# Kernel tuning notes

Hardware: AMD Instinct MI355X
Metric: run time of the kernel (lower is better)

Reference implementation:

```python
import jax, jax.numpy as jnp
import numpy as np

EPS = 1e-6

def setup_inputs() -> dict:
    key = jax.random.key(0)
    M, N, D = 6, 4096, 512
    output = jax.random.normal(key, (M, N, D), dtype=jnp.float32)
    return {"output": output}

def reference(output):
    # output: [M, N, D] stacked per-layer features (already flatten(1)'d)
    M, N, _ = output.shape
    # Gram matrices K_i = X_i @ X_i^T with zeroed diagonal: [M, N, N]
    K = jnp.einsum('ind,imd->inm', output, output)
    K = K * (1.0 - jnp.eye(N, dtype=K.dtype))
    # Double centering H@K@H == K - rowmean - colmean + totalmean
    row = jnp.mean(K, axis=2, keepdims=True)
    col = jnp.mean(K, axis=1, keepdims=True)
    tot = jnp.mean(K, axis=(1, 2), keepdims=True)
    Khat = K - row - col + tot
    # Pairwise HSIC(K_i, K_j) = |sum(Khat_i * Khat_j)| : [M, M]
    S = jnp.abs(jnp.einsum('inm,jnm->ij', Khat, Khat))
    diag = jnp.diagonal(S)
    cka = S / jnp.sqrt(diag[:, None] * diag[None, :] + EPS)
    # Original only fills the strict lower triangle
    hsic_matrix = cka * jnp.tril(jnp.ones((M, M), dtype=cka.dtype), k=-1)
    l = jnp.sum(jnp.abs(hsic_matrix))
    hsic_visual = hsic_matrix + hsic_matrix.T + jnp.eye(M, dtype=cka.dtype)
    return (hsic_visual, l)
```

## Files before the change

### kernel.cpp

```cpp
#include <hip/hip_runtime.h>
#include <hip/hip_bf16.h>
#include <stdint.h>


#define NPTS  4096
#define DF    512
#define ML    6
#define NPAIR 21
#define KSPLIT 8
#define KCHUNK (NPTS / KSPLIT)
#define BK    64

typedef __bf16 bf16_t;
typedef bf16_t bf16x8 __attribute__((ext_vector_type(8)));
typedef float  f32x4  __attribute__((ext_vector_type(4)));
typedef unsigned short u16;
typedef u16 u16x8 __attribute__((ext_vector_type(8)));

__constant__ int c_PI[NPAIR] = {0,0,0,0,0,0, 1,1,1,1,1, 2,2,2,2, 3,3,3, 4,4, 5};
__constant__ int c_PJ[NPAIR] = {0,1,2,3,4,5, 1,2,3,4,5, 2,3,4,5, 3,4,5, 4,5, 5};

#define OFF_XT 0u
#define OFF_S  25165824u
#define OFF_F  (OFF_S + 12288u)
#define OFF_D  (OFF_F + 512u)
#define OFF_XS (OFF_D + 98304u)
#define ZERO_BYTES (12288u + 512u + 98304u + 98304u)
#define OFF_DD (OFF_XS + 98304u)
#define OFF_RD (OFF_DD + 256u)
#define OFF_T  (OFF_RD + 256u)

__device__ __forceinline__ u16 f2bf(float x) {
    union { float f; unsigned u; } v; v.f = x;
    unsigned r = v.u + 0x7fffu + ((v.u >> 16) & 1u);
    return (u16)(r >> 16);
}
__device__ __forceinline__ float bf2f(u16 h) {
    union { unsigned u; float f; } v; v.u = ((unsigned)h) << 16; return v.f;
}

__device__ __forceinline__ void gl2lds16(const void* g, void* l) {
    __builtin_amdgcn_global_load_lds(
        (__attribute__((address_space(1))) void*)g,
        (__attribute__((address_space(3))) void*)l, 16, 0, 0);
}

__global__ __launch_bounds__(256) void k_transpose(const float* __restrict__ X,
                                                   u16* __restrict__ Xt,
                                                   float* __restrict__ s,
                                                   float* __restrict__ dv) {
    __shared__ float tT[64][67];
    int l = blockIdx.z, n0 = blockIdx.x * 64, d0 = blockIdx.y * 64;
    int t = threadIdx.x, q = t & 15, r = t >> 4;
    const float4* src = (const float4*)(X + ((size_t)l * NPTS + n0) * DF + d0);
#pragma unroll
    for (int p = 0; p < 4; ++p) {
        int rr = r + 16 * p;
        float4 v = src[(size_t)rr * (DF / 4) + q];
        tT[4 * q + 0][rr] = v.x;
        tT[4 * q + 1][rr] = v.y;
        tT[4 * q + 2][rr] = v.z;
        tT[4 * q + 3][rr] = v.w;
    }
    __syncthreads();
    if (t < 64) {
        float cs = 0.f;
#pragma unroll
        for (int k = 0; k < 64; ++k) {
            int n = (6 * t + k) & 63;
            cs += tT[t][n];
        }
        atomicAdd(&s[l * DF + d0 + t], cs);
    } else if (t < 128) {
        int n = t - 64;
        float rs = 0.f;
#pragma unroll
        for (int d = 0; d < 64; ++d) { float v = tT[d][n]; rs += v * v; }
        atomicAdd(&dv[l * NPTS + n0 + n], rs);
    }
#pragma unroll
    for (int pp = 0; pp < 2; ++pp) {
        int dcol = (t >> 3) + 32 * pp, n8 = (t & 7) * 8;
        u16x8 o;
#pragma unroll
        for (int j = 0; j < 8; ++j) o[j] = f2bf(tT[dcol][n8 + j]);
        *(u16x8*)(Xt + ((size_t)(l * DF + d0 + dcol)) * NPTS + n0 + n8) = o;
    }
}

__global__ __launch_bounds__(256) void k_rowdot(const u16* __restrict__ Xt,
                                                const float* __restrict__ s,
                                                float* __restrict__ xs) {
    int l = blockIdx.z, d0 = blockIdx.y * 64, n0 = blockIdx.x * 1024;
    int t = threadIdx.x;
    __shared__ float sl[64];
    if (t < 64) sl[t] = s[l * DF + d0 + t];
    __syncthreads();
    const u16* base = Xt + ((size_t)(l * DF + d0)) * NPTS + n0 + t * 4;
    float a0 = 0, a1 = 0, a2 = 0, a3 = 0;
#pragma unroll 8
    for (int d = 0; d < 64; ++d) {
        ushort4 v = *(const ushort4*)(base + (size_t)d * NPTS);
        float sv = sl[d];
        a0 += sv * bf2f(v.x); a1 += sv * bf2f(v.y);
        a2 += sv * bf2f(v.z); a3 += sv * bf2f(v.w);
    }
    float* o = xs + l * NPTS + n0 + t * 4;
    atomicAdd(&o[0], a0); atomicAdd(&o[1], a1);
    atomicAdd(&o[2], a2); atomicAdd(&o[3], a3);
}

__global__ __launch_bounds__(256) void k_pairdots(const float* __restrict__ dv,
                                                  const float* __restrict__ xs,
                                                  const float* __restrict__ s,
                                                  float* __restrict__ ddot,
                                                  float* __restrict__ rdot,
                                                  float* __restrict__ tb) {
    int p = blockIdx.x, i = c_PI[p], j = c_PJ[p];
    int t = threadIdx.x;
    const float invN = 1.0f / (float)NPTS;
    float dd = 0.f, rr = 0.f, sd = 0.f, ss = 0.f;
    for (int n = t; n < NPTS; n += 256) {
        float di = dv[i * NPTS + n], dj = dv[j * NPTS + n];
        float ri = (xs[i * NPTS + n] - di) * invN;
        float rj = (xs[j * NPTS + n] - dj) * invN;
        dd += di * dj;
        rr += ri * rj;
        sd += di;
    }
    for (int c = t; c < DF; c += 256) { float v = s[i * DF + c]; ss += v * v; }
    __shared__ float4 red[256];
    red[t] = make_float4(dd, rr, sd, ss);
    __syncthreads();
    for (int h = 128; h > 0; h >>= 1) {
        if (t < h) {
            float4 a = red[t], b = red[t + h];
            red[t] = make_float4(a.x + b.x, a.y + b.y, a.z + b.z, a.w + b.w);
        }
        __syncthreads();
    }
    if (t == 0) {
        ddot[p] = red[0].x;
        rdot[p] = red[0].y;
        if (i == j)
            tb[i] = (red[0].w - red[0].z) * (1.0f / ((float)NPTS * (float)NPTS));
    }
}

__global__ __launch_bounds__(256, 2) void k_gemm_frob(const u16* __restrict__ Xt,
                                                      float* __restrict__ F) {
    int p = blockIdx.y;
    int aBase = (blockIdx.x & 3) * 128;
    int bBase = (blockIdx.x >> 2) * 256;
    int kLo = blockIdx.z * KCHUNK, kHi = kLo + KCHUNK;
    const u16* A = Xt + ((size_t)(c_PI[p] * DF + aBase)) * NPTS;
    const u16* B = Xt + ((size_t)(c_PJ[p] * DF + bBase)) * NPTS;

    __shared__ __align__(16) u16 As[128 * BK];
    __shared__ __align__(16) u16 Bs[256 * BK];

    int t = threadIdx.x, wave = t >> 6, lane = t & 63;
    int rl = lane >> 3, g = lane & 7;
    int wr = (wave >> 1) * 64, wc = (wave & 1) * 128;
    int row16 = lane & 15, quad = lane >> 4;

    f32x4 acc[4][8];
#pragma unroll
    for (int mi = 0; mi < 4; ++mi)
#pragma unroll
        for (int ni = 0; ni < 8; ++ni) acc[mi][ni] = (f32x4)0.0f;

    for (int k0 = kLo; k0 < kHi; k0 += BK) {
        __syncthreads();
#pragma unroll
        for (int is = 0; is < 4; ++is) {
            int rbase = is * 32 + wave * 8;
            int r = rbase + rl;
            int gs = g ^ (r & 7);
            gl2lds16(A + (size_t)r * NPTS + k0 + gs * 8, &As[rbase * BK]);
        }
#pragma unroll
        for (int is = 0; is < 8; ++is) {
            int rbase = is * 32 + wave * 8;
            int r = rbase + rl;
            int gs = g ^ (r & 7);
            gl2lds16(B + (size_t)r * NPTS + k0 + gs * 8, &Bs[rbase * BK]);
        }
        __syncthreads();

#pragma unroll
        for (int ko = 0; ko < 2; ++ko) {
            bf16x8 af[4], bf[8];
#pragma unroll
            for (int mi = 0; mi < 4; ++mi) {
                int row = wr + mi * 16 + row16;
                int gg = (ko * 4 + quad) ^ (row & 7);
                af[mi] = *(const bf16x8*)&As[row * BK + gg * 8];
            }
#pragma unroll
            for (int ni = 0; ni < 8; ++ni) {
                int row = wc + ni * 16 + row16;
                int gg = (ko * 4 + quad) ^ (row & 7);
                bf[ni] = *(const bf16x8*)&Bs[row * BK + gg * 8];
            }
#pragma unroll
            for (int mi = 0; mi < 4; ++mi)
#pragma unroll
                for (int ni = 0; ni < 8; ++ni)
                    acc[mi][ni] = __builtin_amdgcn_mfma_f32_16x16x32_bf16(
                        af[mi], bf[ni], acc[mi][ni], 0, 0, 0);
        }
    }

    float local = 0.f;
#pragma unroll
    for (int mi = 0; mi < 4; ++mi)
#pragma unroll
        for (int ni = 0; ni < 8; ++ni)
#pragma unroll
            for (int e = 0; e < 4; ++e)
                local += acc[mi][ni][e] * acc[mi][ni][e];
    for (int off = 32; off; off >>= 1) local += __shfl_down(local, off);
    __shared__ float wsum[4];
    if (lane == 0) wsum[wave] = local;
    __syncthreads();
    if (t == 0) atomicAdd(&F[p], wsum[0] + wsum[1] + wsum[2] + wsum[3]);
}

__global__ __launch_bounds__(64) void k_finalize(const float* __restrict__ F,
                                                 const float* __restrict__ ddot,
                                                 const float* __restrict__ rdot,
                                                 const float* __restrict__ tb,
                                                 float* __restrict__ out) {
    __shared__ double hs[ML][ML];
    __shared__ float cka[ML][ML];
    int t = threadIdx.x;
    if (t < NPAIR) {
        int i = c_PI[t], j = c_PJ[t];
        double v = (double)F[t] - (double)ddot[t]
                 - 2.0 * (double)NPTS * (double)rdot[t]
                 + (double)NPTS * (double)NPTS * (double)tb[i] * (double)tb[j];
        hs[i][j] = v; hs[j][i] = v;
    }
    __syncthreads();
    if (t < ML * ML) {
        int i = t / ML, j = t % ML;
        float v;
        if (i == j) v = 1.0f;
        else v = (float)(fabs(hs[i][j]) / sqrt(hs[i][i] * hs[j][j] + 1e-6));
        cka[i][j] = v;
        out[t] = v;
    }
    __syncthreads();
    if (t == 0) {
        float l = 0.f;
        for (int i = 1; i < ML; ++i)
            for (int j = 0; j < i; ++j) l += cka[i][j];
        out[ML * ML] = l;
    }
}

extern "C" void kernel_launch(void* const* d_in, const int* in_sizes, int n_in,
                              void* d_out, int out_size, void* d_ws, size_t ws_size,
                              hipStream_t stream) {
    (void)in_sizes; (void)n_in; (void)out_size; (void)ws_size;
    const float* X = (const float*)d_in[0];
    float* out = (float*)d_out;
    char* ws = (char*)d_ws;
    u16*   Xt = (u16*)(ws + OFF_XT);
    float* s  = (float*)(ws + OFF_S);
    float* F  = (float*)(ws + OFF_F);
    float* dv = (float*)(ws + OFF_D);
    float* xs = (float*)(ws + OFF_XS);
    float* dd = (float*)(ws + OFF_DD);
    float* rd = (float*)(ws + OFF_RD);
    float* tb = (float*)(ws + OFF_T);

    hipMemsetAsync(ws + OFF_S, 0, ZERO_BYTES, stream);

    hipLaunchKernelGGL(k_transpose, dim3(64, 8, 6), dim3(256), 0, stream, X, Xt, s, dv);
    hipLaunchKernelGGL(k_gemm_frob, dim3(8, NPAIR, KSPLIT), dim3(256), 0, stream, Xt, F);
    hipLaunchKernelGGL(k_rowdot,    dim3(4, 8, 6),  dim3(256), 0, stream, Xt, s, xs);
    hipLaunchKernelGGL(k_pairdots,  dim3(NPAIR),    dim3(256), 0, stream, dv, xs, s, dd, rd, tb);
    hipLaunchKernelGGL(k_finalize,  dim3(1),        dim3(64),  0, stream, F, dd, rd, tb, out);
}
```

Measured before the change: 152.8 us.

## Exploit Gram symmetry for same-layer pairs by computing only upper-triangle tiles

The GEMM kernel now uses a flat 1D grid and handles the six same-layer pairs separately. For those pairs it computes only the 10 upper-triangle 128x128 tiles over the full K range, and doubles the Frobenius contribution of the off-diagonal tiles. The 15 cross-layer pairs keep the original split-K 128x256 tiling. This removes redundant MMA work on the symmetric Gram products. In exchange the diagonal blocks are longer-running with smaller, less efficient tiles, which can create load imbalance and a tail.

```diff
diff --git a/kernel.cpp b/kernel.cpp
--- a/kernel.cpp
+++ b/kernel.cpp
@@ -10,6 +10,9 @@
 #define KSPLIT 8
 #define KCHUNK (NPTS / KSPLIT)
 #define BK    64
+#define NDIAGBLK 60
+#define NOFFBLK  960
+#define NGEMMBLK (NDIAGBLK + NOFFBLK)
 
 typedef __bf16 bf16_t;
 typedef bf16_t bf16x8 __attribute__((ext_vector_type(8)));
@@ -19,6 +22,10 @@
 
 __constant__ int c_PI[NPAIR] = {0,0,0,0,0,0, 1,1,1,1,1, 2,2,2,2, 3,3,3, 4,4, 5};
 __constant__ int c_PJ[NPAIR] = {0,1,2,3,4,5, 1,2,3,4,5, 2,3,4,5, 3,4,5, 4,5, 5};
+__constant__ int c_DIAGP[ML]  = {0, 6, 11, 15, 18, 20};
+__constant__ int c_OFFP[15]   = {1,2,3,4,5, 7,8,9,10, 12,13,14, 16,17, 19};
+__constant__ int c_TM[10] = {0,0,0,0, 1,1,1, 2,2, 3};
+__constant__ int c_TN[10] = {0,1,2,3, 1,2,3, 2,3, 3};
 
 #define OFF_XT 0u
 #define OFF_S  25165824u
@@ -149,82 +156,149 @@
 
 __global__ __launch_bounds__(256, 2) void k_gemm_frob(const u16* __restrict__ Xt,
                                                       float* __restrict__ F) {
-    int p = blockIdx.y;
-    int aBase = (blockIdx.x & 3) * 128;
-    int bBase = (blockIdx.x >> 2) * 256;
-    int kLo = blockIdx.z * KCHUNK, kHi = kLo + KCHUNK;
-    const u16* A = Xt + ((size_t)(c_PI[p] * DF + aBase)) * NPTS;
-    const u16* B = Xt + ((size_t)(c_PJ[p] * DF + bBase)) * NPTS;
-
-    __shared__ __align__(16) u16 As[128 * BK];
-    __shared__ __align__(16) u16 Bs[256 * BK];
-
+    int b = blockIdx.x;
     int t = threadIdx.x, wave = t >> 6, lane = t & 63;
     int rl = lane >> 3, g = lane & 7;
-    int wr = (wave >> 1) * 64, wc = (wave & 1) * 128;
     int row16 = lane & 15, quad = lane >> 4;
 
-    f32x4 acc[4][8];
-#pragma unroll
-    for (int mi = 0; mi < 4; ++mi)
-#pragma unroll
-        for (int ni = 0; ni < 8; ++ni) acc[mi][ni] = (f32x4)0.0f;
-
-    for (int k0 = kLo; k0 < kHi; k0 += BK) {
-        __syncthreads();
-#pragma unroll
-        for (int is = 0; is < 4; ++is) {
-            int rbase = is * 32 + wave * 8;
-            int r = rbase + rl;
-            int gs = g ^ (r & 7);
-            gl2lds16(A + (size_t)r * NPTS + k0 + gs * 8, &As[rbase * BK]);
+    float local = 0.f;
+    int pp;
+
+    if (b < NDIAGBLK) {
+        int li = b / 10, tt = b - li * 10;
+        int mt = c_TM[tt], nt = c_TN[tt];
+        const u16* A = Xt + ((size_t)(li * DF + mt * 128)) * NPTS;
+        const u16* B = Xt + ((size_t)(li * DF + nt * 128)) * NPTS;
+        float w = (mt == nt) ? 1.0f : 2.0f;
+        pp = c_DIAGP[li];
+
+        __shared__ __align__(16) u16 As[128 * BK];
+        __shared__ __align__(16) u16 Bs[256 * BK];
+
+        int wr = (wave >> 1) * 64, wc = (wave & 1) * 64;
+        f32x4 acc[4][4];
+#pragma unroll
+        for (int mi = 0; mi < 4; ++mi)
+#pragma unroll
+            for (int ni = 0; ni < 4; ++ni) acc[mi][ni] = (f32x4)0.0f;
+
+        for (int k0 = 0; k0 < NPTS; k0 += BK) {
+            __syncthreads();
+#pragma unroll
+            for (int is = 0; is < 4; ++is) {
+                int rbase = is * 32 + wave * 8;
+                int r = rbase + rl;
+                int gs = g ^ (r & 7);
+                gl2lds16(A + (size_t)r * NPTS + k0 + gs * 8, &As[rbase * BK]);
+                gl2lds16(B + (size_t)r * NPTS + k0 + gs * 8, &Bs[rbase * BK]);
+            }
+            __syncthreads();
+#pragma unroll
+            for (int ko = 0; ko < 2; ++ko) {
+                bf16x8 af[4], bf[4];
+#pragma unroll
+                for (int mi = 0; mi < 4; ++mi) {
+                    int row = wr + mi * 16 + row16;
+                    int gg = (ko * 4 + quad) ^ (row & 7);
+                    af[mi] = *(const bf16x8*)&As[row * BK + gg * 8];
+                }
+#pragma unroll
+                for (int ni = 0; ni < 4; ++ni) {
+                    int row = wc + ni * 16 + row16;
+                    int gg = (ko * 4 + quad) ^ (row & 7);
+                    bf[ni] = *(const bf16x8*)&Bs[row * BK + gg * 8];
+                }
+#pragma unroll
+                for (int mi = 0; mi < 4; ++mi)
+#pragma unroll
+                    for (int ni = 0; ni < 4; ++ni)
+                        acc[mi][ni] = __builtin_amdgcn_mfma_f32_16x16x32_bf16(
+                            af[mi], bf[ni], acc[mi][ni], 0, 0, 0);
+            }
         }
 #pragma unroll
-        for (int is = 0; is < 8; ++is) {
-            int rbase = is * 32 + wave * 8;
-            int r = rbase + rl;
-            int gs = g ^ (r & 7);
-            gl2lds16(B + (size_t)r * NPTS + k0 + gs * 8, &Bs[rbase * BK]);
+        for (int mi = 0; mi < 4; ++mi)
+#pragma unroll
+            for (int ni = 0; ni < 4; ++ni)
+#pragma unroll
+                for (int e = 0; e < 4; ++e)
+                    local += acc[mi][ni][e] * acc[mi][ni][e];
+        local *= w;
+    } else {
+        int b2 = b - NDIAGBLK;
+        int op = b2 >> 6, rem = b2 & 63;
+        int tile = rem >> 3, z = rem & 7;
+        pp = c_OFFP[op];
+        int aBase = (tile & 3) * 128;
+        int bBase = (tile >> 2) * 256;
+        int kLo = z * KCHUNK, kHi = kLo + KCHUNK;
+        const u16* A = Xt + ((size_t)(c_PI[pp] * DF + aBase)) * NPTS;
+        const u16* B = Xt + ((size_t)(c_PJ[pp] * DF + bBase)) * NPTS;
+
+        __shared__ __align__(16) u16 As[128 * BK];
+        __shared__ __align__(16) u16 Bs[256 * BK];
+
+        int wr = (wave >> 1) * 64, wc = (wave & 1) * 128;
+        f32x4 acc[4][8];
+#pragma unroll
+        for (int mi = 0; mi < 4; ++mi)
+#pragma unroll
+            for (int ni = 0; ni < 8; ++ni) acc[mi][ni] = (f32x4)0.0f;
+
+        for (int k0 = kLo; k0 < kHi; k0 += BK) {
+            __syncthreads();
+#pragma unroll
+            for (int is = 0; is < 4; ++is) {
+                int rbase = is * 32 + wave * 8;
+                int r = rbase + rl;
+                int gs = g ^ (r & 7);
+                gl2lds16(A + (size_t)r * NPTS + k0 + gs * 8, &As[rbase * BK]);
+            }
+#pragma unroll
+            for (int is = 0; is < 8; ++is) {
+                int rbase = is * 32 + wave * 8;
+                int r = rbase + rl;
+                int gs = g ^ (r & 7);
+                gl2lds16(B + (size_t)r * NPTS + k0 + gs * 8, &Bs[rbase * BK]);
+            }
+            __syncthreads();
+#pragma unroll
+            for (int ko = 0; ko < 2; ++ko) {
+                bf16x8 af[4], bf[8];
+#pragma unroll
+                for (int mi = 0; mi < 4; ++mi) {
+                    int row = wr + mi * 16 + row16;
+                    int gg = (ko * 4 + quad) ^ (row & 7);
+                    af[mi] = *(const bf16x8*)&As[row * BK + gg * 8];
+                }
+#pragma unroll
+                for (int ni = 0; ni < 8; ++ni) {
+                    int row = wc + ni * 16 + row16;
+                    int gg = (ko * 4 + quad) ^ (row & 7);
+                    bf[ni] = *(const bf16x8*)&Bs[row * BK + gg * 8];
+                }
+#pragma unroll
+                for (int mi = 0; mi < 4; ++mi)
+#pragma unroll
+                    for (int ni = 0; ni < 8; ++ni)
+                        acc[mi][ni] = __builtin_amdgcn_mfma_f32_16x16x32_bf16(
+                            af[mi], bf[ni], acc[mi][ni], 0, 0, 0);
+            }
         }
-        __syncthreads();
-
-#pragma unroll
-        for (int ko = 0; ko < 2; ++ko) {
-            bf16x8 af[4], bf[8];
-#pragma unroll
-            for (int mi = 0; mi < 4; ++mi) {
-                int row = wr + mi * 16 + row16;
-                int gg = (ko * 4 + quad) ^ (row & 7);
-                af[mi] = *(const bf16x8*)&As[row * BK + gg * 8];
-            }
-#pragma unroll
-            for (int ni = 0; ni < 8; ++ni) {
-                int row = wc + ni * 16 + row16;
-                int gg = (ko * 4 + quad) ^ (row & 7);
-                bf[ni] = *(const bf16x8*)&Bs[row * BK + gg * 8];
-            }
-#pragma unroll
-            for (int mi = 0; mi < 4; ++mi)
-#pragma unroll
-                for (int ni = 0; ni < 8; ++ni)
-                    acc[mi][ni] = __builtin_amdgcn_mfma_f32_16x16x32_bf16(
-                        af[mi], bf[ni], acc[mi][ni], 0, 0, 0);
-        }
-    }
-
-    float local = 0.f;
-#pragma unroll
-    for (int mi = 0; mi < 4; ++mi)
-#pragma unroll
-        for (int ni = 0; ni < 8; ++ni)
-#pragma unroll
-            for (int e = 0; e < 4; ++e)
-                local += acc[mi][ni][e] * acc[mi][ni][e];
+#pragma unroll
+        for (int mi = 0; mi < 4; ++mi)
+#pragma unroll
+            for (int ni = 0; ni < 8; ++ni)
+#pragma unroll
+                for (int e = 0; e < 4; ++e)
+                    local += acc[mi][ni][e] * acc[mi][ni][e];
+    }
+
     for (int off = 32; off; off >>= 1) local += __shfl_down(local, off);
     __shared__ float wsum[4];
     if (lane == 0) wsum[wave] = local;
     __syncthreads();
-    if (t == 0) atomicAdd(&F[p], wsum[0] + wsum[1] + wsum[2] + wsum[3]);
+    if (t == 0) atomicAdd(&F[pp], wsum[0] + wsum[1] + wsum[2] + wsum[3]);
 }
 
 __global__ __launch_bounds__(64) void k_finalize(const float* __restrict__ F,
@@ -279,7 +353,7 @@
     hipMemsetAsync(ws + OFF_S, 0, ZERO_BYTES, stream);
 
     hipLaunchKernelGGL(k_transpose, dim3(64, 8, 6), dim3(256), 0, stream, X, Xt, s, dv);
-    hipLaunchKernelGGL(k_gemm_frob, dim3(8, NPAIR, KSPLIT), dim3(256), 0, stream, Xt, F);
+    hipLaunchKernelGGL(k_gemm_frob, dim3(NGEMMBLK), dim3(256), 0, stream, Xt, F);
     hipLaunchKernelGGL(k_rowdot,    dim3(4, 8, 6),  dim3(256), 0, stream, Xt, s, xs);
     hipLaunchKernelGGL(k_pairdots,  dim3(NPAIR),    dim3(256), 0, stream, dv, xs, s, dd, rd, tb);
     hipLaunchKernelGGL(k_finalize,  dim3(1),        dim3(64),  0, stream, F, dd, rd, tb, out);
```

New measurement: 179.6 us. 1.18x slower.
